# Optimization experiments

Hardware: AMD Instinct MI355X
Metric: run time of the kernel (lower is better)

## Reference

```python
import jax, jax.numpy as jnp
import numpy as np

D = 512      # model_dim
H = 8        # num_heads
HD = D // H  # head_dim = 64
S = 196      # tokens per channel (14x14 grid)
CHANNELS = np.array([2, 4, 6, 4], dtype=np.int32)  # multiplex channels per sample


def setup_inputs() -> dict:
    key = jax.random.key(0)
    ks = jax.random.split(key, 8)
    C = int(CHANNELS.sum())  # 16
    n = lambda k, shp, s=1.0: jax.random.normal(k, shp, dtype=jnp.float32) * s
    return {
        "x_query": n(ks[0], (C, S, D)),
        "x_keyval": n(ks[1], (C, S, D)),
        "pos": n(ks[2], (C, S, D)),
        "channels": CHANNELS,
        "Wq": n(ks[3], (D, D), 0.02), "bq": jnp.zeros((D,), jnp.float32),
        "Wk": n(ks[4], (D, D), 0.02), "bk": jnp.zeros((D,), jnp.float32),
        "Wv": n(ks[5], (D, D), 0.02), "bv": jnp.zeros((D,), jnp.float32),
        "Wo": n(ks[6], (D, D), 0.02), "bo": jnp.zeros((D,), jnp.float32),
    }


def reference(x_query, x_keyval, pos, channels, Wq, bq, Wk, bk, Wv, bv, Wo, bo):
    C, S_, D_ = x_query.shape
    ch = np.asarray(channels)
    # segment id per packed token; segment i has length channels[i]*S (== cu_seq_len blocks)
    seg = np.repeat(np.arange(ch.shape[0]), ch * S_)                # [T] static
    block_mask = seg[:, None] == seg[None, :]                        # [T,T] static bool

    xq = x_query.reshape(-1, D_)   # [T,D]
    xk = x_keyval.reshape(-1, D_)
    p = pos.reshape(-1, D_)

    # positional embedding fused into Q/K before projection (query_pos/key_pos)
    q = ((xq + p) @ Wq + bq).reshape(-1, H, HD)
    k = ((xk + p) @ Wk + bk).reshape(-1, H, HD)
    v = (xk @ Wv + bv).reshape(-1, H, HD)

    scale = 1.0 / np.sqrt(HD)
    scores = jnp.einsum('qhd,khd->hqk', q, k) * scale               # [H,T,T]
    scores = jnp.where(block_mask[None], scores, jnp.float32(-1e30))
    attn = jax.nn.softmax(scores, axis=-1)
    out = jnp.einsum('hqk,khd->qhd', attn, v).reshape(-1, D_)       # [T,D]
    out = out @ Wo + bo
    return out.reshape(C, S_, D_)
```

## Files before the change

### kernel.cpp

```cpp
#include <hip/hip_runtime.h>


typedef short short8 __attribute__((ext_vector_type(8)));
typedef float f32x4 __attribute__((ext_vector_type(4)));

__device__ __forceinline__ float b2f(unsigned short u) {
    union { float f; unsigned int i; } x; x.i = ((unsigned int)u) << 16; return x.f;
}
__device__ __forceinline__ unsigned short f2b(float f) {
    union { float f; unsigned int i; } x; x.f = f;
    unsigned int r = x.i + 0x7fffu + ((x.i >> 16) & 1u);
    return (unsigned short)(r >> 16);
}

#define NE 1605632
#define WE 262144

__launch_bounds__(256)
__global__ void prep(const float* __restrict__ xq, const float* __restrict__ xk,
                     const float* __restrict__ pos,
                     const float* __restrict__ W0, const float* __restrict__ W1,
                     const float* __restrict__ W2, const float* __restrict__ W3,
                     unsigned short* __restrict__ WF,
                     unsigned short* __restrict__ aqb, unsigned short* __restrict__ akb,
                     unsigned short* __restrict__ xkbb) {
    const int tid = threadIdx.x;
    if (blockIdx.z < 4) {
        if (blockIdx.x >= 128) return;
        const float* W = blockIdx.z == 0 ? W0 : blockIdx.z == 1 ? W1 : blockIdx.z == 2 ? W2 : W3;
        unsigned short* T = WF + (size_t)blockIdx.z * WE;
        const int s = blockIdx.x * 4 + (tid >> 6);
        const int f = s >> 4, t = s & 15;
        const int lane = tid & 63, quad = lane >> 4, l16 = lane & 15;
        short8 o;
        #pragma unroll
        for (int j = 0; j < 8; ++j)
            o[j] = (short)f2b(W[(size_t)(t * 32 + quad * 8 + j) * 512 + f * 16 + l16]);
        *(short8*)(T + (size_t)s * 512 + lane * 8) = o;
    } else {
        const size_t e = ((size_t)blockIdx.x * 256 + tid) * 8;
        f32x4 q0 = *(const f32x4*)(xq + e),  q1 = *(const f32x4*)(xq + e + 4);
        f32x4 k0 = *(const f32x4*)(xk + e),  k1 = *(const f32x4*)(xk + e + 4);
        f32x4 p0 = *(const f32x4*)(pos + e), p1 = *(const f32x4*)(pos + e + 4);
        short8 a, b, c;
        #pragma unroll
        for (int j = 0; j < 4; ++j) {
            a[j] = (short)f2b(q0[j] + p0[j]); a[4 + j] = (short)f2b(q1[j] + p1[j]);
            b[j] = (short)f2b(k0[j] + p0[j]); b[4 + j] = (short)f2b(k1[j] + p1[j]);
            c[j] = (short)f2b(k0[j]);         c[4 + j] = (short)f2b(k1[j]);
        }
        *(short8*)(aqb + e)  = a;
        *(short8*)(akb + e)  = b;
        *(short8*)(xkbb + e) = c;
    }
}

template <bool OUT_F32>
__device__ __forceinline__ void gemm_wave(const unsigned short* __restrict__ A,
                                          const unsigned short* __restrict__ WFw,
                                          const float* __restrict__ bias,
                                          void* __restrict__ C,
                                          int m0, int n0) {
    const int lane = threadIdx.x & 63;
    const int quad = lane >> 4, l16 = lane & 15;
    const int f0 = n0 >> 4;
    const unsigned short* Arow = A + (size_t)(m0 + l16) * 512 + quad * 8;
    const unsigned short* Bbase = WFw + (size_t)lane * 8;

    f32x4 acc[4] = {};
    #pragma unroll 4
    for (int t = 0; t < 16; ++t) {
        short8 af = *(const short8*)(Arow + t * 32);
        #pragma unroll
        for (int nt = 0; nt < 4; ++nt) {
            short8 bf = *(const short8*)(Bbase + (size_t)((f0 + nt) * 16 + t) * 512);
            acc[nt] = __builtin_amdgcn_mfma_f32_16x16x32_bf16(af, bf, acc[nt], 0, 0, 0);
        }
    }
    #pragma unroll
    for (int nt = 0; nt < 4; ++nt) {
        const int col = n0 + nt * 16 + l16;
        const float bv = bias[col];
        #pragma unroll
        for (int r = 0; r < 4; ++r) {
            const int row = m0 + quad * 4 + r;
            float cv = acc[nt][r] + bv;
            if constexpr (OUT_F32) ((float*)C)[(size_t)row * 512 + col] = cv;
            else ((unsigned short*)C)[(size_t)row * 512 + col] = f2b(cv);
        }
    }
}

__launch_bounds__(256)
__global__ void qkv_gemm(const unsigned short* __restrict__ aqb,
                         const unsigned short* __restrict__ akb,
                         const unsigned short* __restrict__ xkbb,
                         const unsigned short* __restrict__ WF,
                         const float* __restrict__ bq, const float* __restrict__ bk,
                         const float* __restrict__ bv,
                         unsigned short* __restrict__ qb, unsigned short* __restrict__ kb,
                         unsigned short* __restrict__ vb) {
    const unsigned short* A; const unsigned short* WFw; const float* bias; unsigned short* C;
    switch (blockIdx.z) {
        case 0:  A = aqb;  WFw = WF;          bias = bq; C = qb; break;
        case 1:  A = akb;  WFw = WF + WE;     bias = bk; C = kb; break;
        default: A = xkbb; WFw = WF + 2 * WE; bias = bv; C = vb; break;
    }
    const int wave = threadIdx.x >> 6;
    gemm_wave<false>(A, WFw, bias, C, blockIdx.x * 64 + wave * 16, blockIdx.y * 64);
}

__launch_bounds__(256)
__global__ void out_gemm(const unsigned short* __restrict__ A,
                         const unsigned short* __restrict__ WFo,
                         const float* __restrict__ bo, float* __restrict__ out) {
    const int wave = threadIdx.x >> 6;
    gemm_wave<true>(A, WFo, bo, out, blockIdx.x * 64 + wave * 16, blockIdx.y * 64);
}

#define GS 72
__launch_bounds__(256)
__global__ void attn_flat(const unsigned short* __restrict__ q,
                          const unsigned short* __restrict__ k,
                          const unsigned short* __restrict__ v,
                          unsigned short* __restrict__ Opart,
                          float* __restrict__ Lpart) {
    __shared__ __align__(16) unsigned short Ks[64 * GS];
    __shared__ __align__(16) unsigned short Vt[64 * GS];
    __shared__ __align__(16) unsigned short Pb[4][16 * GS];
    const int bx = blockIdx.x, h = blockIdx.y;
    int off, L, qt, ch;
    if (bx < 49)       { off = 0;    L = 392;  qt = bx / 7;  ch = bx - qt * 7; }
    else if (bx < 218) { off = 392;  L = 784;  int i = bx - 49;  qt = i / 13; ch = i - qt * 13; }
    else if (bx < 579) { off = 1176; L = 1176; int i = bx - 218; qt = i / 19; ch = i - qt * 19; }
    else               { off = 2352; L = 784;  int i = bx - 579; qt = i / 13; ch = i - qt * 13; }
    const int tid = threadIdx.x;
    const int wave = tid >> 6, lane = tid & 63;
    const int quad = lane >> 4, l16 = lane & 15;
    const int hb = h * 64;
    const int lastr = off + L - 1;

    int qrow = off + qt * 64 + wave * 16 + l16;
    if (qrow > lastr) qrow = lastr;
    short8 aq0 = *(const short8*)(q + (size_t)qrow * 512 + hb + quad * 8);
    short8 aq1 = *(const short8*)(q + (size_t)qrow * 512 + hb + 32 + quad * 8);

    const int skey = tid & 63, sd = (tid >> 6) * 16;
    {
        int kk = ch * 64 + skey;
        int krow = off + (kk < L ? kk : L - 1);
        short8 kr0 = *(const short8*)(k + (size_t)krow * 512 + hb + sd);
        short8 kr1 = *(const short8*)(k + (size_t)krow * 512 + hb + sd + 8);
        short8 vr0 = *(const short8*)(v + (size_t)krow * 512 + hb + sd);
        short8 vr1 = *(const short8*)(v + (size_t)krow * 512 + hb + sd + 8);
        *(short8*)(Ks + skey * GS + sd)     = kr0;
        *(short8*)(Ks + skey * GS + sd + 8) = kr1;
        #pragma unroll
        for (int j = 0; j < 8; ++j) {
            Vt[(sd + j) * GS + skey]     = (unsigned short)vr0[j];
            Vt[(sd + 8 + j) * GS + skey] = (unsigned short)vr1[j];
        }
    }
    __syncthreads();

    f32x4 s[4];
    #pragma unroll
    for (int g = 0; g < 4; ++g) {
        short8 kb0 = *(const short8*)(Ks + (g * 16 + l16) * GS + quad * 8);
        short8 kb1 = *(const short8*)(Ks + (g * 16 + l16) * GS + 32 + quad * 8);
        f32x4 z = {0.f, 0.f, 0.f, 0.f};
        z = __builtin_amdgcn_mfma_f32_16x16x32_bf16(aq0, kb0, z, 0, 0, 0);
        s[g] = __builtin_amdgcn_mfma_f32_16x16x32_bf16(aq1, kb1, z, 0, 0, 0);
    }
    float p[4][4], lrow[4] = {0.f, 0.f, 0.f, 0.f};
    #pragma unroll
    for (int g = 0; g < 4; ++g) {
        const bool valid = (ch * 64 + g * 16 + l16) < L;
        #pragma unroll
        for (int r = 0; r < 4; ++r) {
            p[g][r] = valid ? __expf(fminf(s[g][r] * 0.125f, 30.f)) : 0.f;
            lrow[r] += p[g][r];
        }
    }
    #pragma unroll
    for (int r = 0; r < 4; ++r) {
        #pragma unroll
        for (int msk = 1; msk < 16; msk <<= 1)
            lrow[r] += __shfl_xor(lrow[r], msk);
    }
    #pragma unroll
    for (int g = 0; g < 4; ++g)
        #pragma unroll
        for (int r = 0; r < 4; ++r)
            Pb[wave][(quad * 4 + r) * GS + g * 16 + l16] = f2b(p[g][r]);
    short8 pa0 = *(const short8*)(Pb[wave] + l16 * GS + quad * 8);
    short8 pa1 = *(const short8*)(Pb[wave] + l16 * GS + 32 + quad * 8);
    f32x4 oacc[4] = {};
    #pragma unroll
    for (int nt = 0; nt < 4; ++nt) {
        short8 vf0 = *(const short8*)(Vt + (nt * 16 + l16) * GS + quad * 8);
        short8 vf1 = *(const short8*)(Vt + (nt * 16 + l16) * GS + 32 + quad * 8);
        oacc[nt] = __builtin_amdgcn_mfma_f32_16x16x32_bf16(pa0, vf0, oacc[nt], 0, 0, 0);
        oacc[nt] = __builtin_amdgcn_mfma_f32_16x16x32_bf16(pa1, vf1, oacc[nt], 0, 0, 0);
    }
    const size_t pidx = (size_t)bx * 8 + h;
    #pragma unroll
    for (int r = 0; r < 4; ++r) {
        const int qi = wave * 16 + quad * 4 + r;
        if (l16 == 0) Lpart[pidx * 64 + qi] = lrow[r];
        #pragma unroll
        for (int nt = 0; nt < 4; ++nt)
            Opart[pidx * 4096 + (size_t)qi * 64 + nt * 16 + l16] = f2b(oacc[nt][r]);
    }
}

__launch_bounds__(256)
__global__ void merge_kernel(const unsigned short* __restrict__ Opart,
                             const float* __restrict__ Lpart,
                             unsigned short* __restrict__ qb) {
    const int e = blockIdx.x * 256 + threadIdx.x;
    const int d8  = (e & 7) * 8;
    const int h   = (e >> 3) & 7;
    const int row = e >> 6;
    int loc, sb, nch;
    if (row < 392)       { loc = row;        sb = 0;   nch = 7;  }
    else if (row < 1176) { loc = row - 392;  sb = 49;  nch = 13; }
    else if (row < 2352) { loc = row - 1176; sb = 218; nch = 19; }
    else                 { loc = row - 2352; sb = 579; nch = 13; }
    const int qt = loc >> 6, r = loc & 63;
    const size_t p0 = ((size_t)(sb + qt * nch)) * 8 + h;

    float ls = 0.f, acc[8] = {};
    for (int c = 0; c < nch; ++c) {
        const size_t pp = p0 + (size_t)c * 8;
        ls += Lpart[pp * 64 + r];
        short8 ov = *(const short8*)(Opart + pp * 4096 + (size_t)r * 64 + d8);
        #pragma unroll
        for (int j = 0; j < 8; ++j) acc[j] += b2f((unsigned short)ov[j]);
    }
    const float inv = 1.0f / ls;
    short8 o;
    #pragma unroll
    for (int j = 0; j < 8; ++j) o[j] = (short)f2b(acc[j] * inv);
    *(short8*)(qb + (size_t)row * 512 + h * 64 + d8) = o;
}

extern "C" void kernel_launch(void* const* d_in, const int* in_sizes, int n_in,
                              void* d_out, int out_size, void* d_ws, size_t ws_size,
                              hipStream_t stream) {
    const float* xq  = (const float*)d_in[0];
    const float* xk  = (const float*)d_in[1];
    const float* pos = (const float*)d_in[2];
    const float* Wq = (const float*)d_in[4];
    const float* bq = (const float*)d_in[5];
    const float* Wk = (const float*)d_in[6];
    const float* bk = (const float*)d_in[7];
    const float* Wv = (const float*)d_in[8];
    const float* bv = (const float*)d_in[9];
    const float* Wo = (const float*)d_in[10];
    const float* bo = (const float*)d_in[11];
    float* out = (float*)d_out;

    unsigned short* ws = (unsigned short*)d_ws;
    unsigned short* qb   = ws;
    unsigned short* kb   = ws + NE;
    unsigned short* vb   = ws + (size_t)2 * NE;
    unsigned short* aqb  = ws + (size_t)3 * NE;
    unsigned short* akb  = ws + (size_t)4 * NE;
    unsigned short* xkbb = ws + (size_t)5 * NE;
    unsigned short* WF   = ws + (size_t)6 * NE;
    float* Lpart = (float*)(ws + (size_t)6 * NE + 4 * WE);
    unsigned short* Opart = ws + (size_t)6 * NE + 4 * WE + 765952;

    prep<<<dim3(784, 1, 5), 256, 0, stream>>>(xq, xk, pos, Wq, Wk, Wv, Wo,
                                              WF, aqb, akb, xkbb);
    qkv_gemm<<<dim3(49, 8, 3), 256, 0, stream>>>(aqb, akb, xkbb, WF, bq, bk, bv,
                                                 qb, kb, vb);
    attn_flat<<<dim3(748, 8), 256, 0, stream>>>(qb, kb, vb, Opart, Lpart);
    merge_kernel<<<dim3(784), 256, 0, stream>>>(Opart, Lpart, qb);
    out_gemm<<<dim3(49, 8), 256, 0, stream>>>(qb, WF + (size_t)3 * WE, bo, out);
}
```

Baseline: 161.3 us.

## Fuse pipeline into one persistent cooperative kernel with grid syncs

Replaces the five separate kernel launches (prep, QKV GEMM, attention, merge, output GEMM) with one cooperative persistent kernel of 512 blocks. Each stage is a grid-stride loop, and stages are separated by grid.sync(). This is meant to remove launch overhead and inter-kernel gaps. The cost is fewer resident blocks than the original grids, the price of a grid-wide barrier at each stage, and possible occupancy limits from launch_bounds(256,2). The old multi-kernel path is kept as a fallback if the cooperative launch fails.

Result: slower. 445.6 us (+176.2%).

```diff
diff --git a/kernel.cpp b/kernel.cpp
--- a/kernel.cpp
+++ b/kernel.cpp
@@ -1,4 +1,7 @@
 #include <hip/hip_runtime.h>
+#include <hip/hip_cooperative_groups.h>
+
+namespace cg = cooperative_groups;
 
 
 typedef short short8 __attribute__((ext_vector_type(8)));
@@ -15,52 +18,61 @@
 
 #define NE 1605632
 #define WE 262144
-
-__launch_bounds__(256)
-__global__ void prep(const float* __restrict__ xq, const float* __restrict__ xk,
-                     const float* __restrict__ pos,
-                     const float* __restrict__ W0, const float* __restrict__ W1,
-                     const float* __restrict__ W2, const float* __restrict__ W3,
-                     unsigned short* __restrict__ WF,
-                     unsigned short* __restrict__ aqb, unsigned short* __restrict__ akb,
-                     unsigned short* __restrict__ xkbb) {
-    const int tid = threadIdx.x;
-    if (blockIdx.z < 4) {
-        if (blockIdx.x >= 128) return;
-        const float* W = blockIdx.z == 0 ? W0 : blockIdx.z == 1 ? W1 : blockIdx.z == 2 ? W2 : W3;
-        unsigned short* T = WF + (size_t)blockIdx.z * WE;
-        const int s = blockIdx.x * 4 + (tid >> 6);
-        const int f = s >> 4, t = s & 15;
-        const int lane = tid & 63, quad = lane >> 4, l16 = lane & 15;
-        short8 o;
-        #pragma unroll
-        for (int j = 0; j < 8; ++j)
-            o[j] = (short)f2b(W[(size_t)(t * 32 + quad * 8 + j) * 512 + f * 16 + l16]);
-        *(short8*)(T + (size_t)s * 512 + lane * 8) = o;
-    } else {
-        const size_t e = ((size_t)blockIdx.x * 256 + tid) * 8;
-        f32x4 q0 = *(const f32x4*)(xq + e),  q1 = *(const f32x4*)(xq + e + 4);
-        f32x4 k0 = *(const f32x4*)(xk + e),  k1 = *(const f32x4*)(xk + e + 4);
-        f32x4 p0 = *(const f32x4*)(pos + e), p1 = *(const f32x4*)(pos + e + 4);
-        short8 a, b, c;
-        #pragma unroll
-        for (int j = 0; j < 4; ++j) {
-            a[j] = (short)f2b(q0[j] + p0[j]); a[4 + j] = (short)f2b(q1[j] + p1[j]);
-            b[j] = (short)f2b(k0[j] + p0[j]); b[4 + j] = (short)f2b(k1[j] + p1[j]);
-            c[j] = (short)f2b(k0[j]);         c[4 + j] = (short)f2b(k1[j]);
-        }
-        *(short8*)(aqb + e)  = a;
-        *(short8*)(akb + e)  = b;
-        *(short8*)(xkbb + e) = c;
-    }
+#define GS 72
+
+#define OFF_QB   ((size_t)0)
+#define OFF_KB   ((size_t)NE)
+#define OFF_VB   ((size_t)2 * NE)
+#define OFF_AQB  ((size_t)3 * NE)
+#define OFF_AKB  ((size_t)4 * NE)
+#define OFF_XKB  ((size_t)5 * NE)
+#define OFF_WF   ((size_t)6 * NE)
+#define OFF_LP   ((size_t)6 * NE + 4 * WE)
+#define OFF_OP   ((size_t)6 * NE + 4 * WE + 765952)
+
+__device__ __forceinline__ void dev_prep_weight(int wjob, int tid,
+                                                const float* W0, const float* W1,
+                                                const float* W2, const float* W3,
+                                                unsigned short* WF) {
+    const int w = wjob >> 9, s = wjob & 511;
+    const float* W = w == 0 ? W0 : w == 1 ? W1 : w == 2 ? W2 : W3;
+    unsigned short* T = WF + (size_t)w * WE;
+    const int f = s >> 4, t = s & 15;
+    const int lane = tid & 63, quad = lane >> 4, l16 = lane & 15;
+    short8 o;
+    #pragma unroll
+    for (int j = 0; j < 8; ++j)
+        o[j] = (short)f2b(W[(size_t)(t * 32 + quad * 8 + j) * 512 + f * 16 + l16]);
+    *(short8*)(T + (size_t)s * 512 + lane * 8) = o;
+}
+
+__device__ __forceinline__ void dev_prep_cast(int j, int tid,
+                                              const float* xq, const float* xk,
+                                              const float* pos,
+                                              unsigned short* aqb, unsigned short* akb,
+                                              unsigned short* xkbb) {
+    const size_t e = ((size_t)j * 256 + tid) * 8;
+    f32x4 q0 = *(const f32x4*)(xq + e),  q1 = *(const f32x4*)(xq + e + 4);
+    f32x4 k0 = *(const f32x4*)(xk + e),  k1 = *(const f32x4*)(xk + e + 4);
+    f32x4 p0 = *(const f32x4*)(pos + e), p1 = *(const f32x4*)(pos + e + 4);
+    short8 a, b, c;
+    #pragma unroll
+    for (int jj = 0; jj < 4; ++jj) {
+        a[jj] = (short)f2b(q0[jj] + p0[jj]); a[4 + jj] = (short)f2b(q1[jj] + p1[jj]);
+        b[jj] = (short)f2b(k0[jj] + p0[jj]); b[4 + jj] = (short)f2b(k1[jj] + p1[jj]);
+        c[jj] = (short)f2b(k0[jj]);          c[4 + jj] = (short)f2b(k1[jj]);
+    }
+    *(short8*)(aqb + e)  = a;
+    *(short8*)(akb + e)  = b;
+    *(short8*)(xkbb + e) = c;
 }
 
 template <bool OUT_F32>
-__device__ __forceinline__ void gemm_wave(const unsigned short* __restrict__ A,
-                                          const unsigned short* __restrict__ WFw,
-                                          const float* __restrict__ bias,
-                                          void* __restrict__ C,
-                                          int m0, int n0) {
+__device__ __forceinline__ void dev_gemm_wave(const unsigned short* __restrict__ A,
+                                              const unsigned short* __restrict__ WFw,
+                                              const float* __restrict__ bias,
+                                              void* __restrict__ C,
+                                              int m0, int n0) {
     const int lane = threadIdx.x & 63;
     const int quad = lane >> 4, l16 = lane & 15;
     const int f0 = n0 >> 4;
@@ -91,44 +103,15 @@
     }
 }
 
-__launch_bounds__(256)
-__global__ void qkv_gemm(const unsigned short* __restrict__ aqb,
-                         const unsigned short* __restrict__ akb,
-                         const unsigned short* __restrict__ xkbb,
-                         const unsigned short* __restrict__ WF,
-                         const float* __restrict__ bq, const float* __restrict__ bk,
-                         const float* __restrict__ bv,
-                         unsigned short* __restrict__ qb, unsigned short* __restrict__ kb,
-                         unsigned short* __restrict__ vb) {
-    const unsigned short* A; const unsigned short* WFw; const float* bias; unsigned short* C;
-    switch (blockIdx.z) {
-        case 0:  A = aqb;  WFw = WF;          bias = bq; C = qb; break;
-        case 1:  A = akb;  WFw = WF + WE;     bias = bk; C = kb; break;
-        default: A = xkbb; WFw = WF + 2 * WE; bias = bv; C = vb; break;
-    }
-    const int wave = threadIdx.x >> 6;
-    gemm_wave<false>(A, WFw, bias, C, blockIdx.x * 64 + wave * 16, blockIdx.y * 64);
-}
-
-__launch_bounds__(256)
-__global__ void out_gemm(const unsigned short* __restrict__ A,
-                         const unsigned short* __restrict__ WFo,
-                         const float* __restrict__ bo, float* __restrict__ out) {
-    const int wave = threadIdx.x >> 6;
-    gemm_wave<true>(A, WFo, bo, out, blockIdx.x * 64 + wave * 16, blockIdx.y * 64);
-}
-
-#define GS 72
-__launch_bounds__(256)
-__global__ void attn_flat(const unsigned short* __restrict__ q,
-                          const unsigned short* __restrict__ k,
-                          const unsigned short* __restrict__ v,
-                          unsigned short* __restrict__ Opart,
-                          float* __restrict__ Lpart) {
+__device__ void dev_attn(int bx, int h,
+                         const unsigned short* __restrict__ q,
+                         const unsigned short* __restrict__ k,
+                         const unsigned short* __restrict__ v,
+                         unsigned short* __restrict__ Opart,
+                         float* __restrict__ Lpart) {
     __shared__ __align__(16) unsigned short Ks[64 * GS];
     __shared__ __align__(16) unsigned short Vt[64 * GS];
     __shared__ __align__(16) unsigned short Pb[4][16 * GS];
-    const int bx = blockIdx.x, h = blockIdx.y;
     int off, L, qt, ch;
     if (bx < 49)       { off = 0;    L = 392;  qt = bx / 7;  ch = bx - qt * 7; }
     else if (bx < 218) { off = 392;  L = 784;  int i = bx - 49;  qt = i / 13; ch = i - qt * 13; }
@@ -145,6 +128,7 @@
     short8 aq0 = *(const short8*)(q + (size_t)qrow * 512 + hb + quad * 8);
     short8 aq1 = *(const short8*)(q + (size_t)qrow * 512 + hb + 32 + quad * 8);
 
+    __syncthreads();
     const int skey = tid & 63, sd = (tid >> 6) * 16;
     {
         int kk = ch * 64 + skey;
@@ -214,11 +198,11 @@
     }
 }
 
-__launch_bounds__(256)
-__global__ void merge_kernel(const unsigned short* __restrict__ Opart,
-                             const float* __restrict__ Lpart,
-                             unsigned short* __restrict__ qb) {
-    const int e = blockIdx.x * 256 + threadIdx.x;
+__device__ __forceinline__ void dev_merge(int j, int tid,
+                                          const unsigned short* __restrict__ Opart,
+                                          const float* __restrict__ Lpart,
+                                          unsigned short* __restrict__ qb) {
+    const int e = j * 256 + tid;
     const int d8  = (e & 7) * 8;
     const int h   = (e >> 3) & 7;
     const int row = e >> 6;
@@ -236,13 +220,104 @@
         ls += Lpart[pp * 64 + r];
         short8 ov = *(const short8*)(Opart + pp * 4096 + (size_t)r * 64 + d8);
         #pragma unroll
-        for (int j = 0; j < 8; ++j) acc[j] += b2f((unsigned short)ov[j]);
+        for (int jj = 0; jj < 8; ++jj) acc[jj] += b2f((unsigned short)ov[jj]);
     }
     const float inv = 1.0f / ls;
     short8 o;
     #pragma unroll
-    for (int j = 0; j < 8; ++j) o[j] = (short)f2b(acc[j] * inv);
+    for (int jj = 0; jj < 8; ++jj) o[jj] = (short)f2b(acc[jj] * inv);
     *(short8*)(qb + (size_t)row * 512 + h * 64 + d8) = o;
+}
+
+__global__ void __launch_bounds__(256, 2)
+mega(const float* xq, const float* xk, const float* pos,
+     const float* Wq, const float* Wk, const float* Wv, const float* Wo,
+     const float* bq, const float* bk, const float* bv, const float* bo,
+     float* out, unsigned short* ws16) {
+    cg::grid_group grid = cg::this_grid();
+    const int bid = blockIdx.x, tid = threadIdx.x, wave = tid >> 6;
+
+    unsigned short* qb   = ws16 + OFF_QB;
+    unsigned short* kb   = ws16 + OFF_KB;
+    unsigned short* vb   = ws16 + OFF_VB;
+    unsigned short* aqb  = ws16 + OFF_AQB;
+    unsigned short* akb  = ws16 + OFF_AKB;
+    unsigned short* xkbb = ws16 + OFF_XKB;
+    unsigned short* WF   = ws16 + OFF_WF;
+    float*          Lp   = (float*)(ws16 + OFF_LP);
+    unsigned short* Op   = ws16 + OFF_OP;
+
+    dev_prep_weight(bid * 4 + wave, tid, Wq, Wk, Wv, Wo, WF);
+    for (int j = bid; j < 784; j += 512) dev_prep_cast(j, tid, xq, xk, pos, aqb, akb, xkbb);
+    grid.sync();
+
+    for (int j = bid; j < 1176; j += 512) {
+        const int mb = j % 49, rest = j / 49, ns = rest & 7, which = rest >> 3;
+        const unsigned short* A   = which == 0 ? aqb : which == 1 ? akb : xkbb;
+        const unsigned short* WFw = WF + (size_t)which * WE;
+        const float* bias         = which == 0 ? bq : which == 1 ? bk : bv;
+        unsigned short* C         = which == 0 ? qb : which == 1 ? kb : vb;
+        dev_gemm_wave<false>(A, WFw, bias, C, mb * 64 + wave * 16, ns * 64);
+    }
+    grid.sync();
+
+    for (int j = bid; j < 5984; j += 512) dev_attn(j >> 3, j & 7, qb, kb, vb, Op, Lp);
+    grid.sync();
+
+    for (int j = bid; j < 784; j += 512) dev_merge(j, tid, Op, Lp, qb);
+    grid.sync();
+
+    for (int j = bid; j < 392; j += 512)
+        dev_gemm_wave<true>(qb, WF + (size_t)3 * WE, bo, out, (j % 49) * 64 + wave * 16,
+                            (j / 49) * 64);
+}
+
+__launch_bounds__(256)
+__global__ void prep_k(const float* xq, const float* xk, const float* pos,
+                       const float* W0, const float* W1, const float* W2, const float* W3,
+                       unsigned short* WF, unsigned short* aqb, unsigned short* akb,
+                       unsigned short* xkbb) {
+    if (blockIdx.z < 4) {
+        if (blockIdx.x >= 128) return;
+        dev_prep_weight(blockIdx.z * 512 + blockIdx.x * 4 + (threadIdx.x >> 6),
+                        threadIdx.x, W0, W1, W2, W3, WF);
+    } else {
+        dev_prep_cast(blockIdx.x, threadIdx.x, xq, xk, pos, aqb, akb, xkbb);
+    }
+}
+
+__launch_bounds__(256)
+__global__ void qkv_k(const unsigned short* aqb, const unsigned short* akb,
+                      const unsigned short* xkbb, const unsigned short* WF,
+                      const float* bq, const float* bk, const float* bv,
+                      unsigned short* qb, unsigned short* kb, unsigned short* vb) {
+    const unsigned short* A; const unsigned short* WFw; const float* bias; unsigned short* C;
+    switch (blockIdx.z) {
+        case 0:  A = aqb;  WFw = WF;          bias = bq; C = qb; break;
+        case 1:  A = akb;  WFw = WF + WE;     bias = bk; C = kb; break;
+        default: A = xkbb; WFw = WF + 2 * WE; bias = bv; C = vb; break;
+    }
+    dev_gemm_wave<false>(A, WFw, bias, C, blockIdx.x * 64 + (threadIdx.x >> 6) * 16,
+                         blockIdx.y * 64);
+}
+
+__launch_bounds__(256)
+__global__ void attn_k(const unsigned short* q, const unsigned short* k,
+                       const unsigned short* v, unsigned short* Opart, float* Lpart) {
+    dev_attn(blockIdx.x, blockIdx.y, q, k, v, Opart, Lpart);
+}
+
+__launch_bounds__(256)
+__global__ void merge_k(const unsigned short* Opart, const float* Lpart,
+                        unsigned short* qb) {
+    dev_merge(blockIdx.x, threadIdx.x, Opart, Lpart, qb);
+}
+
+__launch_bounds__(256)
+__global__ void out_k(const unsigned short* A, const unsigned short* WFo,
+                      const float* bo, float* out) {
+    dev_gemm_wave<true>(A, WFo, bo, out, blockIdx.x * 64 + (threadIdx.x >> 6) * 16,
+                        blockIdx.y * 64);
 }
 
 extern "C" void kernel_launch(void* const* d_in, const int* in_sizes, int n_in,
@@ -260,23 +335,31 @@
     const float* Wo = (const float*)d_in[10];
     const float* bo = (const float*)d_in[11];
     float* out = (float*)d_out;
-
-    unsigned short* ws = (unsigned short*)d_ws;
-    unsigned short* qb   = ws;
-    unsigned short* kb   = ws + NE;
-    unsigned short* vb   = ws + (size_t)2 * NE;
-    unsigned short* aqb  = ws + (size_t)3 * NE;
-    unsigned short* akb  = ws + (size_t)4 * NE;
-    unsigned short* xkbb = ws + (size_t)5 * NE;
-    unsigned short* WF   = ws + (size_t)6 * NE;
-    float* Lpart = (float*)(ws + (size_t)6 * NE + 4 * WE);
-    unsigned short* Opart = ws + (size_t)6 * NE + 4 * WE + 765952;
-
-    prep<<<dim3(784, 1, 5), 256, 0, stream>>>(xq, xk, pos, Wq, Wk, Wv, Wo,
-                                              WF, aqb, akb, xkbb);
-    qkv_gemm<<<dim3(49, 8, 3), 256, 0, stream>>>(aqb, akb, xkbb, WF, bq, bk, bv,
-                                                 qb, kb, vb);
-    attn_flat<<<dim3(748, 8), 256, 0, stream>>>(qb, kb, vb, Opart, Lpart);
-    merge_kernel<<<dim3(784), 256, 0, stream>>>(Opart, Lpart, qb);
-    out_gemm<<<dim3(49, 8), 256, 0, stream>>>(qb, WF + (size_t)3 * WE, bo, out);
-}
+    unsigned short* ws16 = (unsigned short*)d_ws;
+
+    const float* a0 = xq; const float* a1 = xk; const float* a2 = pos;
+    const float* a3 = Wq; const float* a4 = Wk; const float* a5 = Wv; const float* a6 = Wo;
+    const float* a7 = bq; const float* a8 = bk; const float* a9 = bv; const float* a10 = bo;
+    float* a11 = out; unsigned short* a12 = ws16;
+    void* args[13] = {&a0, &a1, &a2, &a3, &a4, &a5, &a6, &a7, &a8, &a9, &a10, &a11, &a12};
+    hipError_t err = hipLaunchCooperativeKernel((void*)mega, dim3(512), dim3(256),
+                                                args, 0, stream);
+    if (err == hipSuccess) return;
+
+    unsigned short* qb   = ws16 + OFF_QB;
+    unsigned short* kb   = ws16 + OFF_KB;
+    unsigned short* vb   = ws16 + OFF_VB;
+    unsigned short* aqb  = ws16 + OFF_AQB;
+    unsigned short* akb  = ws16 + OFF_AKB;
+    unsigned short* xkbb = ws16 + OFF_XKB;
+    unsigned short* WF   = ws16 + OFF_WF;
+    float*          Lp   = (float*)(ws16 + OFF_LP);
+    unsigned short* Op   = ws16 + OFF_OP;
+
+    prep_k<<<dim3(784, 1, 5), 256, 0, stream>>>(xq, xk, pos, Wq, Wk, Wv, Wo,
+                                                WF, aqb, akb, xkbb);
+    qkv_k<<<dim3(49, 8, 3), 256, 0, stream>>>(aqb, akb, xkbb, WF, bq, bk, bv, qb, kb, vb);
+    attn_k<<<dim3(748, 8), 256, 0, stream>>>(qb, kb, vb, Op, Lp);
+    merge_k<<<dim3(784), 256, 0, stream>>>(Op, Lp, qb);
+    out_k<<<dim3(49, 8), 256, 0, stream>>>(qb, WF + (size_t)3 * WE, bo, out);
+}
```

## Fuse split-KV attention and merge into a per-segment key-tile loop

Applied to the files above, without the earlier changes.

Each attention block now loops over every key tile of its segment and accumulates the softmax sum and output in registers. The next tile's K/V is prefetched into registers while the current tile is being computed. The normalized result is written straight into the Q buffer, which removes the partial-output buffers and the separate merge kernel. In exchange the grid shrinks from thousands of blocks to 416, and the longest segment runs 19 tiles serially, so parallelism and latency hiding drop.

New measurement: 153.0 us, median of 2. 5.2% less time.

```diff
diff --git a/kernel.cpp b/kernel.cpp
--- a/kernel.cpp
+++ b/kernel.cpp
@@ -15,6 +15,7 @@
 
 #define NE 1605632
 #define WE 262144
+#define GS 72
 
 __launch_bounds__(256)
 __global__ void prep(const float* __restrict__ xq, const float* __restrict__ xk,
@@ -106,34 +107,32 @@
         case 1:  A = akb;  WFw = WF + WE;     bias = bk; C = kb; break;
         default: A = xkbb; WFw = WF + 2 * WE; bias = bv; C = vb; break;
     }
-    const int wave = threadIdx.x >> 6;
-    gemm_wave<false>(A, WFw, bias, C, blockIdx.x * 64 + wave * 16, blockIdx.y * 64);
+    gemm_wave<false>(A, WFw, bias, C, blockIdx.x * 64 + (threadIdx.x >> 6) * 16,
+                     blockIdx.y * 64);
 }
 
 __launch_bounds__(256)
 __global__ void out_gemm(const unsigned short* __restrict__ A,
                          const unsigned short* __restrict__ WFo,
                          const float* __restrict__ bo, float* __restrict__ out) {
-    const int wave = threadIdx.x >> 6;
-    gemm_wave<true>(A, WFo, bo, out, blockIdx.x * 64 + wave * 16, blockIdx.y * 64);
-}
-
-#define GS 72
-__launch_bounds__(256)
-__global__ void attn_flat(const unsigned short* __restrict__ q,
-                          const unsigned short* __restrict__ k,
-                          const unsigned short* __restrict__ v,
-                          unsigned short* __restrict__ Opart,
-                          float* __restrict__ Lpart) {
+    gemm_wave<true>(A, WFo, bo, out, blockIdx.x * 64 + (threadIdx.x >> 6) * 16,
+                    blockIdx.y * 64);
+}
+
+__launch_bounds__(256)
+__global__ void attn_seg(const unsigned short* __restrict__ q,
+                         const unsigned short* __restrict__ k,
+                         const unsigned short* __restrict__ v,
+                         unsigned short* __restrict__ o) {
     __shared__ __align__(16) unsigned short Ks[64 * GS];
     __shared__ __align__(16) unsigned short Vt[64 * GS];
     __shared__ __align__(16) unsigned short Pb[4][16 * GS];
     const int bx = blockIdx.x, h = blockIdx.y;
-    int off, L, qt, ch;
-    if (bx < 49)       { off = 0;    L = 392;  qt = bx / 7;  ch = bx - qt * 7; }
-    else if (bx < 218) { off = 392;  L = 784;  int i = bx - 49;  qt = i / 13; ch = i - qt * 13; }
-    else if (bx < 579) { off = 1176; L = 1176; int i = bx - 218; qt = i / 19; ch = i - qt * 19; }
-    else               { off = 2352; L = 784;  int i = bx - 579; qt = i / 13; ch = i - qt * 13; }
+    int off, L, qt;
+    if (bx < 7)       { off = 0;    L = 392;  qt = bx; }
+    else if (bx < 20) { off = 392;  L = 784;  qt = bx - 7; }
+    else if (bx < 39) { off = 1176; L = 1176; qt = bx - 20; }
+    else              { off = 2352; L = 784;  qt = bx - 39; }
     const int tid = threadIdx.x;
     const int wave = tid >> 6, lane = tid & 63;
     const int quad = lane >> 4, l16 = lane & 15;
@@ -146,13 +145,21 @@
     short8 aq1 = *(const short8*)(q + (size_t)qrow * 512 + hb + 32 + quad * 8);
 
     const int skey = tid & 63, sd = (tid >> 6) * 16;
+    const int ntiles = (L + 63) >> 6;
+
+    float lrow[4] = {0.f, 0.f, 0.f, 0.f};
+    f32x4 oacc[4] = {};
+
+    short8 kr0, kr1, vr0, vr1;
     {
-        int kk = ch * 64 + skey;
-        int krow = off + (kk < L ? kk : L - 1);
-        short8 kr0 = *(const short8*)(k + (size_t)krow * 512 + hb + sd);
-        short8 kr1 = *(const short8*)(k + (size_t)krow * 512 + hb + sd + 8);
-        short8 vr0 = *(const short8*)(v + (size_t)krow * 512 + hb + sd);
-        short8 vr1 = *(const short8*)(v + (size_t)krow * 512 + hb + sd + 8);
+        int krow = off + skey;
+        kr0 = *(const short8*)(k + (size_t)krow * 512 + hb + sd);
+        kr1 = *(const short8*)(k + (size_t)krow * 512 + hb + sd + 8);
+        vr0 = *(const short8*)(v + (size_t)krow * 512 + hb + sd);
+        vr1 = *(const short8*)(v + (size_t)krow * 512 + hb + sd + 8);
+    }
+    for (int b = 0; b < ntiles; ++b) {
+        __syncthreads();
         *(short8*)(Ks + skey * GS + sd)     = kr0;
         *(short8*)(Ks + skey * GS + sd + 8) = kr1;
         #pragma unroll
@@ -160,26 +167,47 @@
             Vt[(sd + j) * GS + skey]     = (unsigned short)vr0[j];
             Vt[(sd + 8 + j) * GS + skey] = (unsigned short)vr1[j];
         }
-    }
-    __syncthreads();
-
-    f32x4 s[4];
-    #pragma unroll
-    for (int g = 0; g < 4; ++g) {
-        short8 kb0 = *(const short8*)(Ks + (g * 16 + l16) * GS + quad * 8);
-        short8 kb1 = *(const short8*)(Ks + (g * 16 + l16) * GS + 32 + quad * 8);
-        f32x4 z = {0.f, 0.f, 0.f, 0.f};
-        z = __builtin_amdgcn_mfma_f32_16x16x32_bf16(aq0, kb0, z, 0, 0, 0);
-        s[g] = __builtin_amdgcn_mfma_f32_16x16x32_bf16(aq1, kb1, z, 0, 0, 0);
-    }
-    float p[4][4], lrow[4] = {0.f, 0.f, 0.f, 0.f};
-    #pragma unroll
-    for (int g = 0; g < 4; ++g) {
-        const bool valid = (ch * 64 + g * 16 + l16) < L;
-        #pragma unroll
-        for (int r = 0; r < 4; ++r) {
-            p[g][r] = valid ? __expf(fminf(s[g][r] * 0.125f, 30.f)) : 0.f;
-            lrow[r] += p[g][r];
+        __syncthreads();
+        if (b + 1 < ntiles) {
+            int kk = (b + 1) * 64 + skey;
+            int krow = off + (kk < L ? kk : L - 1);
+            kr0 = *(const short8*)(k + (size_t)krow * 512 + hb + sd);
+            kr1 = *(const short8*)(k + (size_t)krow * 512 + hb + sd + 8);
+            vr0 = *(const short8*)(v + (size_t)krow * 512 + hb + sd);
+            vr1 = *(const short8*)(v + (size_t)krow * 512 + hb + sd + 8);
+        }
+        f32x4 s[4];
+        #pragma unroll
+        for (int g = 0; g < 4; ++g) {
+            short8 kb0 = *(const short8*)(Ks + (g * 16 + l16) * GS + quad * 8);
+            short8 kb1 = *(const short8*)(Ks + (g * 16 + l16) * GS + 32 + quad * 8);
+            f32x4 z = {0.f, 0.f, 0.f, 0.f};
+            z = __builtin_amdgcn_mfma_f32_16x16x32_bf16(aq0, kb0, z, 0, 0, 0);
+            s[g] = __builtin_amdgcn_mfma_f32_16x16x32_bf16(aq1, kb1, z, 0, 0, 0);
+        }
+        float p[4][4];
+        #pragma unroll
+        for (int g = 0; g < 4; ++g) {
+            const bool valid = (b * 64 + g * 16 + l16) < L;
+            #pragma unroll
+            for (int r = 0; r < 4; ++r) {
+                p[g][r] = valid ? __expf(fminf(s[g][r] * 0.125f, 30.f)) : 0.f;
+                lrow[r] += p[g][r];
+            }
+        }
+        #pragma unroll
+        for (int g = 0; g < 4; ++g)
+            #pragma unroll
+            for (int r = 0; r < 4; ++r)
+                Pb[wave][(quad * 4 + r) * GS + g * 16 + l16] = f2b(p[g][r]);
+        short8 pa0 = *(const short8*)(Pb[wave] + l16 * GS + quad * 8);
+        short8 pa1 = *(const short8*)(Pb[wave] + l16 * GS + 32 + quad * 8);
+        #pragma unroll
+        for (int nt = 0; nt < 4; ++nt) {
+            short8 vf0 = *(const short8*)(Vt + (nt * 16 + l16) * GS + quad * 8);
+            short8 vf1 = *(const short8*)(Vt + (nt * 16 + l16) * GS + 32 + quad * 8);
+            oacc[nt] = __builtin_amdgcn_mfma_f32_16x16x32_bf16(pa0, vf0, oacc[nt], 0, 0, 0);
+            oacc[nt] = __builtin_amdgcn_mfma_f32_16x16x32_bf16(pa1, vf1, oacc[nt], 0, 0, 0);
         }
     }
     #pragma unroll
@@ -188,61 +216,18 @@
         for (int msk = 1; msk < 16; msk <<= 1)
             lrow[r] += __shfl_xor(lrow[r], msk);
     }
-    #pragma unroll
-    for (int g = 0; g < 4; ++g)
-        #pragma unroll
-        for (int r = 0; r < 4; ++r)
-            Pb[wave][(quad * 4 + r) * GS + g * 16 + l16] = f2b(p[g][r]);
-    short8 pa0 = *(const short8*)(Pb[wave] + l16 * GS + quad * 8);
-    short8 pa1 = *(const short8*)(Pb[wave] + l16 * GS + 32 + quad * 8);
-    f32x4 oacc[4] = {};
+    float linv[4];
+    #pragma unroll
+    for (int r = 0; r < 4; ++r) linv[r] = 1.0f / lrow[r];
     #pragma unroll
     for (int nt = 0; nt < 4; ++nt) {
-        short8 vf0 = *(const short8*)(Vt + (nt * 16 + l16) * GS + quad * 8);
-        short8 vf1 = *(const short8*)(Vt + (nt * 16 + l16) * GS + 32 + quad * 8);
-        oacc[nt] = __builtin_amdgcn_mfma_f32_16x16x32_bf16(pa0, vf0, oacc[nt], 0, 0, 0);
-        oacc[nt] = __builtin_amdgcn_mfma_f32_16x16x32_bf16(pa1, vf1, oacc[nt], 0, 0, 0);
-    }
-    const size_t pidx = (size_t)bx * 8 + h;
-    #pragma unroll
-    for (int r = 0; r < 4; ++r) {
-        const int qi = wave * 16 + quad * 4 + r;
-        if (l16 == 0) Lpart[pidx * 64 + qi] = lrow[r];
-        #pragma unroll
-        for (int nt = 0; nt < 4; ++nt)
-            Opart[pidx * 4096 + (size_t)qi * 64 + nt * 16 + l16] = f2b(oacc[nt][r]);
-    }
-}
-
-__launch_bounds__(256)
-__global__ void merge_kernel(const unsigned short* __restrict__ Opart,
-                             const float* __restrict__ Lpart,
-                             unsigned short* __restrict__ qb) {
-    const int e = blockIdx.x * 256 + threadIdx.x;
-    const int d8  = (e & 7) * 8;
-    const int h   = (e >> 3) & 7;
-    const int row = e >> 6;
-    int loc, sb, nch;
-    if (row < 392)       { loc = row;        sb = 0;   nch = 7;  }
-    else if (row < 1176) { loc = row - 392;  sb = 49;  nch = 13; }
-    else if (row < 2352) { loc = row - 1176; sb = 218; nch = 19; }
-    else                 { loc = row - 2352; sb = 579; nch = 13; }
-    const int qt = loc >> 6, r = loc & 63;
-    const size_t p0 = ((size_t)(sb + qt * nch)) * 8 + h;
-
-    float ls = 0.f, acc[8] = {};
-    for (int c = 0; c < nch; ++c) {
-        const size_t pp = p0 + (size_t)c * 8;
-        ls += Lpart[pp * 64 + r];
-        short8 ov = *(const short8*)(Opart + pp * 4096 + (size_t)r * 64 + d8);
-        #pragma unroll
-        for (int j = 0; j < 8; ++j) acc[j] += b2f((unsigned short)ov[j]);
-    }
-    const float inv = 1.0f / ls;
-    short8 o;
-    #pragma unroll
-    for (int j = 0; j < 8; ++j) o[j] = (short)f2b(acc[j] * inv);
-    *(short8*)(qb + (size_t)row * 512 + h * 64 + d8) = o;
+        #pragma unroll
+        for (int r = 0; r < 4; ++r) {
+            const int qi = qt * 64 + wave * 16 + quad * 4 + r;
+            if (qi < L)
+                o[(size_t)(off + qi) * 512 + hb + nt * 16 + l16] = f2b(oacc[nt][r] * linv[r]);
+        }
+    }
 }
 
 extern "C" void kernel_launch(void* const* d_in, const int* in_sizes, int n_in,
@@ -269,14 +254,11 @@
     unsigned short* akb  = ws + (size_t)4 * NE;
     unsigned short* xkbb = ws + (size_t)5 * NE;
     unsigned short* WF   = ws + (size_t)6 * NE;
-    float* Lpart = (float*)(ws + (size_t)6 * NE + 4 * WE);
-    unsigned short* Opart = ws + (size_t)6 * NE + 4 * WE + 765952;
 
     prep<<<dim3(784, 1, 5), 256, 0, stream>>>(xq, xk, pos, Wq, Wk, Wv, Wo,
                                               WF, aqb, akb, xkbb);
     qkv_gemm<<<dim3(49, 8, 3), 256, 0, stream>>>(aqb, akb, xkbb, WF, bq, bk, bv,
                                                  qb, kb, vb);
-    attn_flat<<<dim3(748, 8), 256, 0, stream>>>(qb, kb, vb, Opart, Lpart);
-    merge_kernel<<<dim3(784), 256, 0, stream>>>(Opart, Lpart, qb);
+    attn_seg<<<dim3(52, 8), 256, 0, stream>>>(qb, kb, vb, qb);
     out_gemm<<<dim3(49, 8), 256, 0, stream>>>(qb, WF + (size_t)3 * WE, bo, out);
 }
```
